# Performance work log

Hardware: AMD Instinct MI355X
Metric: run time of the kernel (lower is better)

Reference implementation:

```python
import jax, jax.numpy as jnp
import numpy as np
import math

B, T, C = 2, 2048, 2048
H, KV, HD = 16, 4, 128          # n_head, n_kv_head, head_dim
REP = H // KV
FFN = 5632                      # multiple_of-rounded 2/3 * 4 * n_embd
EPS = 1e-5


def setup_inputs() -> dict:
    key = jax.random.key(0)
    ks = jax.random.split(key, 10)
    s = 0.02
    x = jax.random.normal(ks[0], (B, T, C), dtype=jnp.float32)
    # RoPE table: (T, HD/2, 2) = (cos, sin)
    inv_freq = 1.0 / (10000.0 ** (np.arange(0, HD, 2, dtype=np.float32) / HD))
    ang = np.arange(T, dtype=np.float32)[:, None] * inv_freq[None, :]
    freqs_cis = jnp.asarray(np.stack([np.cos(ang), np.sin(ang)], axis=-1))
    wq = s * jax.random.normal(ks[1], (H * HD, C), dtype=jnp.float32)
    wk = s * jax.random.normal(ks[2], (KV * HD, C), dtype=jnp.float32)
    wv = s * jax.random.normal(ks[3], (KV * HD, C), dtype=jnp.float32)
    wo = s * jax.random.normal(ks[4], (C, H * HD), dtype=jnp.float32)
    w1 = s * jax.random.normal(ks[5], (FFN, C), dtype=jnp.float32)
    w2 = s * jax.random.normal(ks[6], (FFN, C), dtype=jnp.float32)
    c_proj = s * jax.random.normal(ks[7], (C, FFN), dtype=jnp.float32)
    g1 = jnp.ones((C,), dtype=jnp.float32)
    g2 = jnp.ones((C,), dtype=jnp.float32)
    return {"x": x, "freqs_cis": freqs_cis, "wq": wq, "wk": wk, "wv": wv,
            "wo": wo, "w1": w1, "w2": w2, "c_proj": c_proj, "g1": g1, "g2": g2}


def _rmsnorm(x, g, eps=EPS):
    return x * jax.lax.rsqrt(jnp.mean(x * x, axis=-1, keepdims=True) + eps) * g


def _rope(t, freqs_cis):
    # t: (B, T, nH, HD); freqs_cis: (T, HD/2, 2)
    tr = t.reshape(*t.shape[:-1], HD // 2, 2)
    cos = freqs_cis[None, :, None, :, 0]
    sin = freqs_cis[None, :, None, :, 1]
    out = jnp.stack([tr[..., 0] * cos - tr[..., 1] * sin,
                     tr[..., 0] * sin + tr[..., 1] * cos], axis=-1)
    return out.reshape(t.shape)


def reference(x, freqs_cis, wq, wk, wv, wo, w1, w2, c_proj, g1, g2):
    h = _rmsnorm(x, g1)
    q = (h @ wq.T).reshape(B, T, H, HD)
    k = (h @ wk.T).reshape(B, T, KV, HD)
    v = (h @ wv.T).reshape(B, T, KV, HD)
    q = _rope(q, freqs_cis)
    k = _rope(k, freqs_cis)
    # GQA: group query heads by kv head; never materialize expanded K/V
    q = q.transpose(0, 2, 1, 3).reshape(B, KV, REP, T, HD)  # b g r q d
    k = k.transpose(0, 2, 1, 3)                              # b g k d
    v = v.transpose(0, 2, 1, 3)                              # b g k d
    scale = 1.0 / math.sqrt(HD)
    scores = jnp.einsum('bgrqd,bgkd->bgrqk', q, k) * scale
    causal = jnp.tril(jnp.ones((T, T), dtype=bool))
    scores = jnp.where(causal, scores, jnp.float32(-1e30))
    attn = jax.nn.softmax(scores, axis=-1)
    y = jnp.einsum('bgrqk,bgkd->bgrqd', attn, v)
    y = y.reshape(B, H, T, HD).transpose(0, 2, 1, 3).reshape(B, T, C)
    x = x + y @ wo.T
    h2 = _rmsnorm(x, g2)
    mlp = (jax.nn.silu(h2 @ w1.T) * (h2 @ w2.T)) @ c_proj.T
    return x + mlp
```

## Files before the change

kernel.cpp:

```cpp
#include <hip/hip_runtime.h>
#include <hip/hip_bf16.h>
#include <math.h>

#define TT   2048
#define CC   2048
#define NB   2
#define NH   16
#define NKV  4
#define HDIM 128
#define NFFN 5632

typedef __attribute__((ext_vector_type(8))) short     bf8;
typedef __attribute__((ext_vector_type(4))) float     f32x4;
typedef __attribute__((ext_vector_type(8))) unsigned short u16x8;
typedef __attribute__((ext_vector_type(4))) unsigned short u16x4;

__device__ __forceinline__ float b2f(unsigned short u) {
    union { unsigned u; float f; } v; v.u = ((unsigned)u) << 16; return v.f;
}
__device__ __forceinline__ unsigned short f2bf(float f) {
    union { float f; unsigned u; } v; v.f = f;
    unsigned r = (v.u + 0x7fffu + ((v.u >> 16) & 1u)) >> 16;
    return (unsigned short)r;
}
__device__ __forceinline__ void gll16(const void* g, void* l) {
    __builtin_amdgcn_global_load_lds((const __attribute__((address_space(1))) void*)g,
                                     (__attribute__((address_space(3))) void*)l, 16, 0, 0);
}

__global__ __launch_bounds__(256) void cvt_k(const float* __restrict__ in,
        __hip_bfloat16* __restrict__ out)
{
    const size_t i = ((size_t)blockIdx.x * 256 + threadIdx.x) * 8;
    float4 a = *(const float4*)(in + i);
    float4 b = *(const float4*)(in + i + 4);
    u16x8 v;
    v[0] = f2bf(a.x); v[1] = f2bf(a.y); v[2] = f2bf(a.z); v[3] = f2bf(a.w);
    v[4] = f2bf(b.x); v[5] = f2bf(b.y); v[6] = f2bf(b.z); v[7] = f2bf(b.w);
    *(u16x8*)((unsigned short*)out + i) = v;
}

__global__ __launch_bounds__(256) void rms_f32_k(const float* __restrict__ x,
        const float* __restrict__ g, __hip_bfloat16* __restrict__ o)
{
    const size_t row = blockIdx.x;
    const int e0 = threadIdx.x * 8;
    float4 a = *(const float4*)(x + row * CC + e0);
    float4 b = *(const float4*)(x + row * CC + e0 + 4);
    float vals[8] = {a.x, a.y, a.z, a.w, b.x, b.y, b.z, b.w};
    float s = 0.f;
    #pragma unroll
    for (int e = 0; e < 8; ++e) s += vals[e] * vals[e];
    #pragma unroll
    for (int off = 32; off; off >>= 1) s += __shfl_xor(s, off);
    __shared__ float wsum[4];
    if ((threadIdx.x & 63) == 0) wsum[threadIdx.x >> 6] = s;
    __syncthreads();
    float scale = rsqrtf((wsum[0] + wsum[1] + wsum[2] + wsum[3]) * (1.0f / CC) + 1e-5f);
    float4 g0 = *(const float4*)(g + e0);
    float4 g1 = *(const float4*)(g + e0 + 4);
    float gs[8] = {g0.x, g0.y, g0.z, g0.w, g1.x, g1.y, g1.z, g1.w};
    u16x8 ov;
    #pragma unroll
    for (int e = 0; e < 8; ++e) ov[e] = f2bf(vals[e] * scale * gs[e]);
    *(u16x8*)((unsigned short*)o + row * CC + e0) = ov;
}

__global__ __launch_bounds__(256) void rms_bf16_k(const __hip_bfloat16* __restrict__ x,
        const float* __restrict__ g, __hip_bfloat16* __restrict__ o)
{
    const size_t row = blockIdx.x;
    const int e0 = threadIdx.x * 8;
    u16x8 xv = *(const u16x8*)((const unsigned short*)x + row * CC + e0);
    float vals[8];
    #pragma unroll
    for (int e = 0; e < 8; ++e) vals[e] = b2f(xv[e]);
    float s = 0.f;
    #pragma unroll
    for (int e = 0; e < 8; ++e) s += vals[e] * vals[e];
    #pragma unroll
    for (int off = 32; off; off >>= 1) s += __shfl_xor(s, off);
    __shared__ float wsum[4];
    if ((threadIdx.x & 63) == 0) wsum[threadIdx.x >> 6] = s;
    __syncthreads();
    float scale = rsqrtf((wsum[0] + wsum[1] + wsum[2] + wsum[3]) * (1.0f / CC) + 1e-5f);
    float4 g0 = *(const float4*)(g + e0);
    float4 g1 = *(const float4*)(g + e0 + 4);
    float gs[8] = {g0.x, g0.y, g0.z, g0.w, g1.x, g1.y, g1.z, g1.w};
    u16x8 ov;
    #pragma unroll
    for (int e = 0; e < 8; ++e) ov[e] = f2bf(vals[e] * scale * gs[e]);
    *(u16x8*)((unsigned short*)o + row * CC + e0) = ov;
}

__global__ __launch_bounds__(256) void rope_k(__hip_bfloat16* __restrict__ t,
        const float* __restrict__ fc, int nh)
{
    const int e = blockIdx.x * 256 + threadIdx.x;
    const int per_row = nh * 64;
    const int row = e / per_row;
    const int rem = e - row * per_row;
    const int hh = rem >> 6, i = rem & 63;
    const int tt = row & (TT - 1);
    const float c = fc[tt * HDIM + i * 2];
    const float s = fc[tt * HDIM + i * 2 + 1];
    unsigned short* p = (unsigned short*)t + (size_t)row * (nh * HDIM) + hh * HDIM + i * 2;
    float a = b2f(p[0]), b = b2f(p[1]);
    p[0] = f2bf(a * c - b * s);
    p[1] = f2bf(a * s + b * c);
}

#define GBM 128
#define GBN 128
#define GBK 32

template<int EPI, int OUTB>
__global__ __launch_bounds__(256) void gemm_db(
        const __hip_bfloat16* __restrict__ A,
        const __hip_bfloat16* __restrict__ W,
        const void* __restrict__ Rp,
        void* __restrict__ Cp,
        int M, int N, int K)
{
    __shared__ alignas(16) __hip_bfloat16 As[2][GBM][GBK];
    __shared__ alignas(16) __hip_bfloat16 Ws[2][GBN][GBK];
    const int tid  = threadIdx.x;
    const int lane = tid & 63;
    const int wid  = tid >> 6;
    const int wr = wid >> 1, wc = wid & 1;
    const int nwg = gridDim.x * gridDim.y;
    const int lin = blockIdx.y * gridDim.x + blockIdx.x;
    const int nlin = (lin & 7) * (nwg >> 3) + (lin >> 3);
    const int bxs = nlin % gridDim.x, bys = nlin / gridDim.x;
    const int bm = bys * GBM, bn = bxs * GBN;
    const int l4  = lane >> 2;
    const int lk8 = (lane & 3) * 8;
    const int fr  = lane & 15;
    const int fk  = (lane >> 4) * 8;

    f32x4 acc[4][4];
    #pragma unroll
    for (int m = 0; m < 4; ++m)
        #pragma unroll
        for (int n = 0; n < 4; ++n) acc[m][n] = (f32x4){0.f, 0.f, 0.f, 0.f};

    const __hip_bfloat16* ga0 = A + (size_t)(bm + wid * 32 + l4) * K + lk8;
    const __hip_bfloat16* ga1 = A + (size_t)(bm + wid * 32 + 16 + l4) * K + lk8;
    const __hip_bfloat16* gw0 = W + (size_t)(bn + wid * 32 + l4) * K + lk8;
    const __hip_bfloat16* gw1 = W + (size_t)(bn + wid * 32 + 16 + l4) * K + lk8;

    const int nt = K >> 5;
    gll16(ga0, &As[0][wid * 32][0]);
    gll16(ga1, &As[0][wid * 32 + 16][0]);
    gll16(gw0, &Ws[0][wid * 32][0]);
    gll16(gw1, &Ws[0][wid * 32 + 16][0]);

    #pragma unroll 2
    for (int t = 0; t < nt; ++t) {
        const int cur = t & 1;
        __syncthreads();
        if (t + 1 < nt) {
            const int k1 = (t + 1) << 5;
            const int nx = cur ^ 1;
            gll16(ga0 + k1, &As[nx][wid * 32][0]);
            gll16(ga1 + k1, &As[nx][wid * 32 + 16][0]);
            gll16(gw0 + k1, &Ws[nx][wid * 32][0]);
            gll16(gw1 + k1, &Ws[nx][wid * 32 + 16][0]);
        }
        bf8 af[4];
        #pragma unroll
        for (int m = 0; m < 4; ++m)
            af[m] = *(const bf8*)&As[cur][wr * 64 + m * 16 + fr][fk];
        #pragma unroll
        for (int n = 0; n < 4; ++n) {
            bf8 wf = *(const bf8*)&Ws[cur][wc * 64 + n * 16 + fr][fk];
            #pragma unroll
            for (int m = 0; m < 4; ++m)
                acc[m][n] = __builtin_amdgcn_mfma_f32_16x16x32_bf16(af[m], wf, acc[m][n], 0, 0, 0);
        }
    }

    const int rj = (lane >> 4) * 4;
    #pragma unroll
    for (int m = 0; m < 4; ++m) {
        #pragma unroll
        for (int j = 0; j < 4; ++j) {
            const size_t row = (size_t)(bm + wr * 64 + m * 16 + rj + j);
            #pragma unroll
            for (int n = 0; n < 4; ++n) {
                const size_t col = (size_t)(bn + wc * 64 + n * 16 + fr);
                float v = acc[m][n][j];
                if (EPI == 1) v += ((const float*)Rp)[row * N + col];
                if (EPI == 2) v += b2f(((const unsigned short*)Rp)[row * N + col]);
                if (EPI == 3) {
                    float gv = b2f(((const unsigned short*)Rp)[row * N + col]);
                    v = (gv / (1.0f + __expf(-gv))) * v;
                }
                if (OUTB) ((unsigned short*)Cp)[row * N + col] = f2bf(v);
                else      ((float*)Cp)[row * N + col] = v;
            }
        }
    }
}

__global__ __launch_bounds__(256) void gemm_qkv_db(
        const __hip_bfloat16* __restrict__ A,
        const __hip_bfloat16* __restrict__ W,
        __hip_bfloat16* __restrict__ qo,
        __hip_bfloat16* __restrict__ ko,
        __hip_bfloat16* __restrict__ vto,
        int M, int K)
{
    __shared__ alignas(16) __hip_bfloat16 As[2][GBM][GBK];
    __shared__ alignas(16) __hip_bfloat16 Ws[2][GBN][GBK];
    const int tid  = threadIdx.x;
    const int lane = tid & 63;
    const int wid  = tid >> 6;
    const int wr = wid >> 1, wc = wid & 1;
    const int nwg = gridDim.x * gridDim.y;
    const int lin = blockIdx.y * gridDim.x + blockIdx.x;
    const int nlin = (lin & 7) * (nwg >> 3) + (lin >> 3);
    const int bxs = nlin % gridDim.x, bys = nlin / gridDim.x;
    const int bm = bys * GBM, bn = bxs * GBN;
    const int l4  = lane >> 2;
    const int lk8 = (lane & 3) * 8;
    const int fr  = lane & 15;
    const int fk  = (lane >> 4) * 8;

    f32x4 acc[4][4];
    #pragma unroll
    for (int m = 0; m < 4; ++m)
        #pragma unroll
        for (int n = 0; n < 4; ++n) acc[m][n] = (f32x4){0.f, 0.f, 0.f, 0.f};

    const __hip_bfloat16* ga0 = A + (size_t)(bm + wid * 32 + l4) * K + lk8;
    const __hip_bfloat16* ga1 = A + (size_t)(bm + wid * 32 + 16 + l4) * K + lk8;
    const __hip_bfloat16* gw0 = W + (size_t)(bn + wid * 32 + l4) * K + lk8;
    const __hip_bfloat16* gw1 = W + (size_t)(bn + wid * 32 + 16 + l4) * K + lk8;

    const int nt = K >> 5;
    gll16(ga0, &As[0][wid * 32][0]);
    gll16(ga1, &As[0][wid * 32 + 16][0]);
    gll16(gw0, &Ws[0][wid * 32][0]);
    gll16(gw1, &Ws[0][wid * 32 + 16][0]);

    #pragma unroll 2
    for (int t = 0; t < nt; ++t) {
        const int cur = t & 1;
        __syncthreads();
        if (t + 1 < nt) {
            const int k1 = (t + 1) << 5;
            const int nx = cur ^ 1;
            gll16(ga0 + k1, &As[nx][wid * 32][0]);
            gll16(ga1 + k1, &As[nx][wid * 32 + 16][0]);
            gll16(gw0 + k1, &Ws[nx][wid * 32][0]);
            gll16(gw1 + k1, &Ws[nx][wid * 32 + 16][0]);
        }
        bf8 af[4];
        #pragma unroll
        for (int m = 0; m < 4; ++m)
            af[m] = *(const bf8*)&As[cur][wr * 64 + m * 16 + fr][fk];
        #pragma unroll
        for (int n = 0; n < 4; ++n) {
            bf8 wf = *(const bf8*)&Ws[cur][wc * 64 + n * 16 + fr][fk];
            #pragma unroll
            for (int m = 0; m < 4; ++m)
                acc[m][n] = __builtin_amdgcn_mfma_f32_16x16x32_bf16(af[m], wf, acc[m][n], 0, 0, 0);
        }
    }

    const int rj = (lane >> 4) * 4;
    #pragma unroll
    for (int m = 0; m < 4; ++m) {
        #pragma unroll
        for (int n = 0; n < 4; ++n) {
            const int col = bn + wc * 64 + n * 16 + fr;
            const int row0 = bm + wr * 64 + m * 16 + rj;
            if (col < 2048) {
                #pragma unroll
                for (int j = 0; j < 4; ++j)
                    ((unsigned short*)qo)[(size_t)(row0 + j) * CC + col] = f2bf(acc[m][n][j]);
            } else if (col < 2560) {
                #pragma unroll
                for (int j = 0; j < 4; ++j)
                    ((unsigned short*)ko)[(size_t)(row0 + j) * (NKV * HDIM) + (col - 2048)] = f2bf(acc[m][n][j]);
            } else {
                const int vc = col - 2560;
                const int g = vc >> 7, d = vc & 127;
                const int b = row0 >> 11, t0 = row0 & (TT - 1);
                unsigned short* vp = (unsigned short*)vto +
                    ((size_t)(b * NKV + g) * HDIM + d) * TT + t0;
                u16x4 ov;
                #pragma unroll
                for (int j = 0; j < 4; ++j) ov[j] = f2bf(acc[m][n][j]);
                *(u16x4*)vp = ov;
            }
        }
    }
}

#define PBM 128
#define PBN 256
#define PBK 64

template<int EPI, int OUTB>
__global__ __launch_bounds__(512) void gemm_8p(
        const __hip_bfloat16* __restrict__ A,
        const __hip_bfloat16* __restrict__ W,
        const void* __restrict__ Rp,
        void* __restrict__ Cp,
        int M, int N, int K)
{
    __shared__ alignas(16) __hip_bfloat16 As[2][PBM][PBK];
    __shared__ alignas(16) __hip_bfloat16 Ws[2][PBN][PBK];
    const int tid  = threadIdx.x;
    const int lane = tid & 63;
    const int wid  = tid >> 6;
    const int wr = wid >> 2, wc = wid & 3;
    const int nwg = gridDim.x * gridDim.y;
    const int lin = blockIdx.y * gridDim.x + blockIdx.x;
    const int nlin = (lin & 7) * (nwg >> 3) + (lin >> 3);
    const int bxs = nlin % gridDim.x, bys = nlin / gridDim.x;
    const int bm = bys * PBM, bn = bxs * PBN;
    const int fr = lane & 15;
    const int hi = lane >> 4;

    f32x4 acc[4][4];
    #pragma unroll
    for (int m = 0; m < 4; ++m)
        #pragma unroll
        for (int n = 0; n < 4; ++n) acc[m][n] = (f32x4){0.f, 0.f, 0.f, 0.f};

    const unsigned short* Ag = (const unsigned short*)A;
    const unsigned short* Wg = (const unsigned short*)W;

    auto STAGE = [&](int buf, int k0) {
        #pragma unroll
        for (int l = 0; l < 2; ++l) {
            const int s = l * 512 + tid;
            const int row = s >> 3;
            const int srcb = ((s & 7) * 16) ^ ((row & 7) << 4);
            gll16(Ag + (size_t)(bm + row) * K + k0 + (srcb >> 1),
                  (unsigned short*)&As[buf][0][0] + (l * 512 + wid * 64) * 8);
        }
        #pragma unroll
        for (int l = 0; l < 4; ++l) {
            const int s = l * 512 + tid;
            const int row = s >> 3;
            const int srcb = ((s & 7) * 16) ^ ((row & 7) << 4);
            gll16(Wg + (size_t)(bn + row) * K + k0 + (srcb >> 1),
                  (unsigned short*)&Ws[buf][0][0] + (l * 512 + wid * 64) * 8);
        }
    };

    const int nt = K >> 6;
    STAGE(0, 0);
    __syncthreads();

    for (int t = 0; t < nt; ++t) {
        const int cur = t & 1;
        const char* Ab = (const char*)&As[cur][0][0];
        const char* Bb = (const char*)&Ws[cur][0][0];

        bf8 bF[4][2];
        #pragma unroll
        for (int n = 0; n < 4; ++n) {
            const int row = wc * 64 + n * 16 + fr;
            #pragma unroll
            for (int kk = 0; kk < 2; ++kk) {
                const int off = (kk * 64 + hi * 16) ^ ((row & 7) << 4);
                bF[n][kk] = *(const bf8*)(Bb + row * 128 + off);
            }
        }
        bf8 a0, a1;
        {
            const int row = wr * 64 + fr;
            a0 = *(const bf8*)(Ab + row * 128 + ((hi * 16)      ^ ((row & 7) << 4)));
            a1 = *(const bf8*)(Ab + row * 128 + ((64 + hi * 16) ^ ((row & 7) << 4)));
        }
        if (t + 1 < nt) STAGE(cur ^ 1, (t + 1) * PBK);
        __builtin_amdgcn_s_barrier();
        __builtin_amdgcn_s_setprio(1);
        #pragma unroll
        for (int n = 0; n < 4; ++n) {
            acc[0][n] = __builtin_amdgcn_mfma_f32_16x16x32_bf16(a0, bF[n][0], acc[0][n], 0, 0, 0);
            acc[0][n] = __builtin_amdgcn_mfma_f32_16x16x32_bf16(a1, bF[n][1], acc[0][n], 0, 0, 0);
        }
        __builtin_amdgcn_s_setprio(0);
        __builtin_amdgcn_s_barrier();

        #pragma unroll
        for (int m = 1; m < 4; ++m) {
            const int row = wr * 64 + m * 16 + fr;
            bf8 am0 = *(const bf8*)(Ab + row * 128 + ((hi * 16)      ^ ((row & 7) << 4)));
            bf8 am1 = *(const bf8*)(Ab + row * 128 + ((64 + hi * 16) ^ ((row & 7) << 4)));
            __builtin_amdgcn_s_barrier();
            __builtin_amdgcn_s_setprio(1);
            #pragma unroll
            for (int n = 0; n < 4; ++n) {
                acc[m][n] = __builtin_amdgcn_mfma_f32_16x16x32_bf16(am0, bF[n][0], acc[m][n], 0, 0, 0);
                acc[m][n] = __builtin_amdgcn_mfma_f32_16x16x32_bf16(am1, bF[n][1], acc[m][n], 0, 0, 0);
            }
            __builtin_amdgcn_s_setprio(0);
            if (m < 3) __builtin_amdgcn_s_barrier();
        }
        __syncthreads();
    }

    const int rj = hi * 4;
    #pragma unroll
    for (int m = 0; m < 4; ++m) {
        #pragma unroll
        for (int j = 0; j < 4; ++j) {
            const size_t row = (size_t)(bm + wr * 64 + m * 16 + rj + j);
            #pragma unroll
            for (int n = 0; n < 4; ++n) {
                const size_t col = (size_t)(bn + wc * 64 + n * 16 + fr);
                float v = acc[m][n][j];
                if (EPI == 1) v += ((const float*)Rp)[row * N + col];
                if (EPI == 2) v += b2f(((const unsigned short*)Rp)[row * N + col]);
                if (EPI == 3) {
                    float gv = b2f(((const unsigned short*)Rp)[row * N + col]);
                    v = (gv / (1.0f + __expf(-gv))) * v;
                }
                if (OUTB) ((unsigned short*)Cp)[row * N + col] = f2bf(v);
                else      ((float*)Cp)[row * N + col] = v;
            }
        }
    }
}

#define AQB 128
#define AKV 64

__global__ __launch_bounds__(512) void attn_mfma(const __hip_bfloat16* __restrict__ q,
        const __hip_bfloat16* __restrict__ k, const __hip_bfloat16* __restrict__ vt,
        __hip_bfloat16* __restrict__ y)
{
    __shared__ alignas(16) unsigned short Ks[AKV * HDIM];
    __shared__ alignas(16) unsigned short Vs[HDIM * AKV];
    __shared__ alignas(16) unsigned short Ps[AQB * AKV];

    const int qt = (TT / AQB - 1) - blockIdx.x;
    const int h  = blockIdx.y;
    const int b  = blockIdx.z;
    const int g  = h >> 2;
    const int qbase = qt * AQB;

    const int tid  = threadIdx.x;
    const int lane = tid & 63;
    const int wid  = tid >> 6;
    const int fr   = lane & 15;
    const int fk8  = (lane >> 4) * 8;
    const int rj   = (lane >> 4) * 4;

    bf8 qf[4];
    {
        const unsigned short* qp = (const unsigned short*)q +
            (size_t)(b * TT + qbase + wid * 16 + fr) * CC + h * HDIM;
        #pragma unroll
        for (int c = 0; c < 4; ++c)
            qf[c] = *(const bf8*)(qp + c * 32 + fk8);
    }
    const unsigned short* vtb = (const unsigned short*)vt + (size_t)(b * NKV + g) * HDIM * TT;

    f32x4 oacc[8];
    float m_r[4], l_r[4];
    #pragma unroll
    for (int n = 0; n < 8; ++n) oacc[n] = (f32x4){0.f, 0.f, 0.f, 0.f};
    #pragma unroll
    for (int j = 0; j < 4; ++j) { m_r[j] = -1e30f; l_r[j] = 0.f; }

    const float scale = 0.08838834764831845f;
    const int ntiles = qbase / AKV + 2;
    const int kjr = tid >> 3;
    const int kkc = (tid & 7) * 16;
    const int vdr = tid >> 2;
    const int vjc = (tid & 3) * 16;

    for (int tile = 0; tile < ntiles; ++tile) {
        const int jbase = tile * AKV;
        __syncthreads();
        {
            const unsigned short* kp = (const unsigned short*)k +
                ((size_t)(b * TT + jbase + kjr) * (NKV * HDIM)) + g * HDIM + kkc;
            const unsigned short* vp = vtb + (size_t)vdr * TT + jbase + vjc;
            #pragma unroll
            for (int c = 0; c < 2; ++c) {
                u16x8 kv = *(const u16x8*)(kp + c * 8);
                const int byteK = (kjr * 256 + (kkc + c * 8) * 2) ^ ((kjr & 7) << 4);
                *(u16x8*)((char*)Ks + byteK) = kv;
                u16x8 vv = *(const u16x8*)(vp + c * 8);
                const int byteV = (vdr * 128 + (vjc + c * 8) * 2) ^ ((vdr & 7) << 4);
                *(u16x8*)((char*)Vs + byteV) = vv;
            }
        }
        __syncthreads();

        f32x4 s[4];
        #pragma unroll
        for (int n = 0; n < 4; ++n) s[n] = (f32x4){0.f, 0.f, 0.f, 0.f};
        __builtin_amdgcn_s_setprio(1);
        #pragma unroll
        for (int c = 0; c < 4; ++c) {
            #pragma unroll
            for (int n = 0; n < 4; ++n) {
                const int j = n * 16 + fr;
                const int byteB = (j * 256 + (c * 32 + fk8) * 2) ^ ((j & 7) << 4);
                bf8 kf = *(const bf8*)((char*)Ks + byteB);
                s[n] = __builtin_amdgcn_mfma_f32_16x16x32_bf16(qf[c], kf, s[n], 0, 0, 0);
            }
        }
        __builtin_amdgcn_s_setprio(0);

        #pragma unroll
        for (int jj = 0; jj < 4; ++jj) {
            const int qg = qbase + wid * 16 + rj + jj;
            float sv[4];
            #pragma unroll
            for (int n = 0; n < 4; ++n) {
                const int jg = jbase + n * 16 + fr;
                sv[n] = (jg <= qg) ? s[n][jj] * scale : -1e30f;
            }
            float tmax = fmaxf(fmaxf(sv[0], sv[1]), fmaxf(sv[2], sv[3]));
            tmax = fmaxf(tmax, __shfl_xor(tmax, 1));
            tmax = fmaxf(tmax, __shfl_xor(tmax, 2));
            tmax = fmaxf(tmax, __shfl_xor(tmax, 4));
            tmax = fmaxf(tmax, __shfl_xor(tmax, 8));
            const float mnew = fmaxf(m_r[jj], tmax);
            const float alpha = __expf(m_r[jj] - mnew);
            m_r[jj] = mnew;
            const int prow = wid * 16 + rj + jj;
            float tsum = 0.f;
            #pragma unroll
            for (int n = 0; n < 4; ++n) {
                const float p = __expf(sv[n] - mnew);
                tsum += p;
                const int byteP = (prow * 128 + (n * 16 + fr) * 2) ^ ((prow & 7) << 4);
                *(unsigned short*)((char*)Ps + byteP) = f2bf(p);
            }
            tsum += __shfl_xor(tsum, 1);
            tsum += __shfl_xor(tsum, 2);
            tsum += __shfl_xor(tsum, 4);
            tsum += __shfl_xor(tsum, 8);
            l_r[jj] = l_r[jj] * alpha + tsum;
            #pragma unroll
            for (int n = 0; n < 8; ++n) oacc[n][jj] *= alpha;
        }

        __builtin_amdgcn_s_setprio(1);
        #pragma unroll
        for (int c2 = 0; c2 < 2; ++c2) {
            const int prow = wid * 16 + fr;
            const int byteA = (prow * 128 + (c2 * 32 + fk8) * 2) ^ ((prow & 7) << 4);
            bf8 pf = *(const bf8*)((char*)Ps + byteA);
            #pragma unroll
            for (int n = 0; n < 8; ++n) {
                const int d = n * 16 + fr;
                const int byteB = (d * 128 + (c2 * 32 + fk8) * 2) ^ ((d & 7) << 4);
                bf8 vf = *(const bf8*)((char*)Vs + byteB);
                oacc[n] = __builtin_amdgcn_mfma_f32_16x16x32_bf16(pf, vf, oacc[n], 0, 0, 0);
            }
        }
        __builtin_amdgcn_s_setprio(0);
    }

    #pragma unroll
    for (int jj = 0; jj < 4; ++jj) {
        const float inv = 1.0f / l_r[jj];
        unsigned short* yrow = (unsigned short*)y +
            ((size_t)(b * TT + qbase + wid * 16 + rj + jj) * CC) + h * HDIM;
        #pragma unroll
        for (int n = 0; n < 8; ++n)
            yrow[n * 16 + fr] = f2bf(oacc[n][jj] * inv);
    }
}

extern "C" void kernel_launch(void* const* d_in, const int* in_sizes, int n_in,
                              void* d_out, int out_size, void* d_ws, size_t ws_size,
                              hipStream_t stream)
{
    (void)in_sizes; (void)n_in; (void)out_size; (void)ws_size;
    const float* x     = (const float*)d_in[0];
    const float* fc    = (const float*)d_in[1];
    const float* wq    = (const float*)d_in[2];
    const float* wk    = (const float*)d_in[3];
    const float* wv    = (const float*)d_in[4];
    const float* wo    = (const float*)d_in[5];
    const float* w1    = (const float*)d_in[6];
    const float* w2    = (const float*)d_in[7];
    const float* cproj = (const float*)d_in[8];
    const float* g1    = (const float*)d_in[9];
    const float* g2    = (const float*)d_in[10];
    float* out = (float*)d_out;

    const int ROWS = NB * TT;
    unsigned char* wsb = (unsigned char*)d_ws;
    __hip_bfloat16* x2b = (__hip_bfloat16*)(wsb);
    __hip_bfloat16* hb  = (__hip_bfloat16*)(wsb + 16777216u);
    __hip_bfloat16* w1b = (__hip_bfloat16*)(wsb + 33554432u);
    __hip_bfloat16* w2b = (__hip_bfloat16*)(wsb + 56623104u);
    __hip_bfloat16* G1  = (__hip_bfloat16*)(wsb + 79691776u);
    __hip_bfloat16* cpb = w1b;
    __hip_bfloat16* qb   = (__hip_bfloat16*)(wsb + 33554432u);
    __hip_bfloat16* kb   = (__hip_bfloat16*)(wsb + 50331648u);
    __hip_bfloat16* vtb  = (__hip_bfloat16*)(wsb + 54525952u);
    __hip_bfloat16* yb   = (__hip_bfloat16*)(wsb + 58720256u);
    __hip_bfloat16* wbuf = (__hip_bfloat16*)(wsb + 75497472u);

    rms_f32_k<<<ROWS, 256, 0, stream>>>(x, g1, hb);
    cvt_k<<<(CC * CC) / 2048, 256, 0, stream>>>(wq, wbuf);
    cvt_k<<<(NKV * HDIM * CC) / 2048, 256, 0, stream>>>(wk, wbuf + (size_t)2048 * CC);
    cvt_k<<<(NKV * HDIM * CC) / 2048, 256, 0, stream>>>(wv, wbuf + (size_t)2560 * CC);
    gemm_qkv_db<<<dim3(3072 / GBN, ROWS / GBM), 256, 0, stream>>>(hb, wbuf, qb, kb, vtb, ROWS, CC);
    rope_k<<<(ROWS * NH * 64) / 256, 256, 0, stream>>>(qb, fc, NH);
    rope_k<<<(ROWS * NKV * 64) / 256, 256, 0, stream>>>(kb, fc, NKV);
    attn_mfma<<<dim3(TT / AQB, NH, NB), 512, 0, stream>>>(qb, kb, vtb, yb);
    cvt_k<<<(CC * CC) / 2048, 256, 0, stream>>>(wo, wbuf);
    gemm_db<1, 1><<<dim3(CC / GBN, ROWS / GBM), 256, 0, stream>>>(yb, wbuf, x, x2b, ROWS, CC, CC);
    rms_bf16_k<<<ROWS, 256, 0, stream>>>(x2b, g2, hb);
    cvt_k<<<(NFFN * CC) / 2048, 256, 0, stream>>>(w1, w1b);
    cvt_k<<<(NFFN * CC) / 2048, 256, 0, stream>>>(w2, w2b);
    gemm_8p<0, 1><<<dim3(NFFN / PBN, ROWS / PBM), 512, 0, stream>>>(hb, w1b, nullptr, G1, ROWS, NFFN, CC);
    gemm_8p<3, 1><<<dim3(NFFN / PBN, ROWS / PBM), 512, 0, stream>>>(hb, w2b, G1, G1, ROWS, NFFN, CC);
    cvt_k<<<(CC * NFFN) / 2048, 256, 0, stream>>>(cproj, cpb);
    gemm_8p<2, 0><<<dim3(CC / PBN, ROWS / PBM), 512, 0, stream>>>(G1, cpb, x2b, out, ROWS, CC, NFFN);
}
```

Before: 686.2 us.

## Fuse RoPE into QKV GEMM epilogue and double-buffer K/V tiles in attention

Applies the rotary embedding directly in the QKV GEMM epilogue, pairing adjacent columns through a lane shuffle, and drops the two separate rope kernel launches along with their extra read-modify-write of Q and K. In attention, K/V tiles are prefetched into registers and written to a second shared-memory buffer, so global loads overlap compute and one barrier per tile goes away. This doubles the K/V shared memory and raises register pressure, which may lower occupancy. RoPE now rotates fp32 accumulators before the bf16 rounding, so numerics shift slightly.

```diff
diff --git a/kernel.cpp b/kernel.cpp
--- a/kernel.cpp
+++ b/kernel.cpp
@@ -91,23 +91,6 @@
     #pragma unroll
     for (int e = 0; e < 8; ++e) ov[e] = f2bf(vals[e] * scale * gs[e]);
     *(u16x8*)((unsigned short*)o + row * CC + e0) = ov;
-}
-
-__global__ __launch_bounds__(256) void rope_k(__hip_bfloat16* __restrict__ t,
-        const float* __restrict__ fc, int nh)
-{
-    const int e = blockIdx.x * 256 + threadIdx.x;
-    const int per_row = nh * 64;
-    const int row = e / per_row;
-    const int rem = e - row * per_row;
-    const int hh = rem >> 6, i = rem & 63;
-    const int tt = row & (TT - 1);
-    const float c = fc[tt * HDIM + i * 2];
-    const float s = fc[tt * HDIM + i * 2 + 1];
-    unsigned short* p = (unsigned short*)t + (size_t)row * (nh * HDIM) + hh * HDIM + i * 2;
-    float a = b2f(p[0]), b = b2f(p[1]);
-    p[0] = f2bf(a * c - b * s);
-    p[1] = f2bf(a * s + b * c);
 }
 
 #define GBM 128
@@ -206,6 +189,7 @@
 __global__ __launch_bounds__(256) void gemm_qkv_db(
         const __hip_bfloat16* __restrict__ A,
         const __hip_bfloat16* __restrict__ W,
+        const float* __restrict__ fc,
         __hip_bfloat16* __restrict__ qo,
         __hip_bfloat16* __restrict__ ko,
         __hip_bfloat16* __restrict__ vto,
@@ -276,14 +260,22 @@
         for (int n = 0; n < 4; ++n) {
             const int col = bn + wc * 64 + n * 16 + fr;
             const int row0 = bm + wr * 64 + m * 16 + rj;
-            if (col < 2048) {
+            if (col < 2560) {
+                const int i2 = ((col & 127) >> 1) * 2;
+                const int role = col & 1;
                 #pragma unroll
-                for (int j = 0; j < 4; ++j)
-                    ((unsigned short*)qo)[(size_t)(row0 + j) * CC + col] = f2bf(acc[m][n][j]);
-            } else if (col < 2560) {
-                #pragma unroll
-                for (int j = 0; j < 4; ++j)
-                    ((unsigned short*)ko)[(size_t)(row0 + j) * (NKV * HDIM) + (col - 2048)] = f2bf(acc[m][n][j]);
+                for (int j = 0; j < 4; ++j) {
+                    const int t0 = (row0 + j) & (TT - 1);
+                    const float cv = fc[t0 * HDIM + i2];
+                    const float sv = fc[t0 * HDIM + i2 + 1];
+                    const float v = acc[m][n][j];
+                    const float partner = __shfl_xor(v, 1);
+                    const float o = role ? (partner * sv + v * cv) : (v * cv - partner * sv);
+                    if (col < 2048)
+                        ((unsigned short*)qo)[(size_t)(row0 + j) * CC + col] = f2bf(o);
+                    else
+                        ((unsigned short*)ko)[(size_t)(row0 + j) * (NKV * HDIM) + (col - 2048)] = f2bf(o);
+                }
             } else {
                 const int vc = col - 2560;
                 const int g = vc >> 7, d = vc & 127;
@@ -437,8 +429,8 @@
         const __hip_bfloat16* __restrict__ k, const __hip_bfloat16* __restrict__ vt,
         __hip_bfloat16* __restrict__ y)
 {
-    __shared__ alignas(16) unsigned short Ks[AKV * HDIM];
-    __shared__ alignas(16) unsigned short Vs[HDIM * AKV];
+    __shared__ alignas(16) unsigned short Ks[2][AKV * HDIM];
+    __shared__ alignas(16) unsigned short Vs[2][HDIM * AKV];
     __shared__ alignas(16) unsigned short Ps[AQB * AKV];
 
     const int qt = (TT / AQB - 1) - blockIdx.x;
@@ -478,23 +470,33 @@
     const int vdr = tid >> 2;
     const int vjc = (tid & 3) * 16;
 
+    u16x8 krg[2], vrg[2];
+    auto LOADT = [&](int jb) {
+        const unsigned short* kp = (const unsigned short*)k +
+            ((size_t)(b * TT + jb + kjr) * (NKV * HDIM)) + g * HDIM + kkc;
+        const unsigned short* vp = vtb + (size_t)vdr * TT + jb + vjc;
+        #pragma unroll
+        for (int c = 0; c < 2; ++c) {
+            krg[c] = *(const u16x8*)(kp + c * 8);
+            vrg[c] = *(const u16x8*)(vp + c * 8);
+        }
+    };
+    auto WRITET = [&](int buf) {
+        #pragma unroll
+        for (int c = 0; c < 2; ++c) {
+            const int byteK = (kjr * 256 + (kkc + c * 8) * 2) ^ ((kjr & 7) << 4);
+            *(u16x8*)((char*)&Ks[buf][0] + byteK) = krg[c];
+            const int byteV = (vdr * 128 + (vjc + c * 8) * 2) ^ ((vdr & 7) << 4);
+            *(u16x8*)((char*)&Vs[buf][0] + byteV) = vrg[c];
+        }
+    };
+
+    LOADT(0);
+    WRITET(0);
+
     for (int tile = 0; tile < ntiles; ++tile) {
-        const int jbase = tile * AKV;
-        __syncthreads();
-        {
-            const unsigned short* kp = (const unsigned short*)k +
-                ((size_t)(b * TT + jbase + kjr) * (NKV * HDIM)) + g * HDIM + kkc;
-            const unsigned short* vp = vtb + (size_t)vdr * TT + jbase + vjc;
-            #pragma unroll
-            for (int c = 0; c < 2; ++c) {
-                u16x8 kv = *(const u16x8*)(kp + c * 8);
-                const int byteK = (kjr * 256 + (kkc + c * 8) * 2) ^ ((kjr & 7) << 4);
-                *(u16x8*)((char*)Ks + byteK) = kv;
-                u16x8 vv = *(const u16x8*)(vp + c * 8);
-                const int byteV = (vdr * 128 + (vjc + c * 8) * 2) ^ ((vdr & 7) << 4);
-                *(u16x8*)((char*)Vs + byteV) = vv;
-            }
-        }
+        const int cur = tile & 1;
+        if (tile + 1 < ntiles) LOADT((tile + 1) * AKV);
         __syncthreads();
 
         f32x4 s[4];
@@ -507,12 +509,13 @@
             for (int n = 0; n < 4; ++n) {
                 const int j = n * 16 + fr;
                 const int byteB = (j * 256 + (c * 32 + fk8) * 2) ^ ((j & 7) << 4);
-                bf8 kf = *(const bf8*)((char*)Ks + byteB);
+                bf8 kf = *(const bf8*)((char*)&Ks[cur][0] + byteB);
                 s[n] = __builtin_amdgcn_mfma_f32_16x16x32_bf16(qf[c], kf, s[n], 0, 0, 0);
             }
         }
         __builtin_amdgcn_s_setprio(0);
 
+        const int jbase = tile * AKV;
         #pragma unroll
         for (int jj = 0; jj < 4; ++jj) {
             const int qg = qbase + wid * 16 + rj + jj;
@@ -558,11 +561,13 @@
             for (int n = 0; n < 8; ++n) {
                 const int d = n * 16 + fr;
                 const int byteB = (d * 128 + (c2 * 32 + fk8) * 2) ^ ((d & 7) << 4);
-                bf8 vf = *(const bf8*)((char*)Vs + byteB);
+                bf8 vf = *(const bf8*)((char*)&Vs[cur][0] + byteB);
                 oacc[n] = __builtin_amdgcn_mfma_f32_16x16x32_bf16(pf, vf, oacc[n], 0, 0, 0);
             }
         }
         __builtin_amdgcn_s_setprio(0);
+
+        if (tile + 1 < ntiles) WRITET(cur ^ 1);
     }
 
     #pragma unroll
@@ -612,9 +617,7 @@
     cvt_k<<<(CC * CC) / 2048, 256, 0, stream>>>(wq, wbuf);
     cvt_k<<<(NKV * HDIM * CC) / 2048, 256, 0, stream>>>(wk, wbuf + (size_t)2048 * CC);
     cvt_k<<<(NKV * HDIM * CC) / 2048, 256, 0, stream>>>(wv, wbuf + (size_t)2560 * CC);
-    gemm_qkv_db<<<dim3(3072 / GBN, ROWS / GBM), 256, 0, stream>>>(hb, wbuf, qb, kb, vtb, ROWS, CC);
-    rope_k<<<(ROWS * NH * 64) / 256, 256, 0, stream>>>(qb, fc, NH);
-    rope_k<<<(ROWS * NKV * 64) / 256, 256, 0, stream>>>(kb, fc, NKV);
+    gemm_qkv_db<<<dim3(3072 / GBN, ROWS / GBM), 256, 0, stream>>>(hb, wbuf, fc, qb, kb, vtb, ROWS, CC);
     attn_mfma<<<dim3(TT / AQB, NH, NB), 512, 0, stream>>>(qb, kb, vtb, yb);
     cvt_k<<<(CC * CC) / 2048, 256, 0, stream>>>(wo, wbuf);
     gemm_db<1, 1><<<dim3(CC / GBN, ROWS / GBM), 256, 0, stream>>>(yb, wbuf, x, x2b, ROWS, CC, CC);
```

Measured after the change: 675.4 us. About the same (-1.6%).
